# Kernel tuning notes

Measured on AMD Instinct MI355X. Metric: run time of the kernel, lower is better.

The kernel has to match this reference:

```python
import jax, jax.numpy as jnp
import numpy as np

B, S, D = 4, 4096, 256


def setup_inputs() -> dict:
    key = jax.random.key(0)
    ks = jax.random.split(key, 8)
    scale = 1.0 / np.sqrt(D)
    inp = {
        "q": jax.random.normal(ks[0], (B, S, D), jnp.float32),
        "k": jax.random.normal(ks[1], (B, S, D), jnp.float32),
        "v": jax.random.normal(ks[2], (B, S, D), jnp.float32),
        # additive mask: 1 where attention is disallowed (causal), broadcast over batch
        "mask": jnp.triu(jnp.ones((S, S), jnp.float32), k=1)[None, :, :],
        "Wq": jax.random.normal(ks[3], (D, D), jnp.float32) * scale,
        "bq": jnp.zeros((D,), jnp.float32),
        "Wk": jax.random.normal(ks[4], (D, D), jnp.float32) * scale,
        "bk": jnp.zeros((D,), jnp.float32),
        "Wv": jax.random.normal(ks[5], (D, D), jnp.float32) * scale,
        "bv": jnp.zeros((D,), jnp.float32),
        "Wo": jax.random.normal(ks[6], (D, D), jnp.float32) * scale,
        "bo": jnp.zeros((D,), jnp.float32),
    }
    return inp


def reference(q, k, v, mask, Wq, bq, Wk, bk, Wv, bv, Wo, bo):
    # Dense projections (Keras Dense: x @ W + b)
    qp = q @ Wq + bq  # [B,S,D]
    kp = k @ Wk + bk
    vp = v @ Wv + bv
    dk = jnp.asarray(qp.shape[-1], qp.dtype)
    # scaled dot-product attention, materialized scores as in the source
    logits = jnp.einsum("bqd,bkd->bqk", qp, kp) / jnp.sqrt(dk)  # [B,S,S]
    logits = logits + mask * (-1e9)
    attn = jax.nn.softmax(logits, axis=-1)  # [B,S,S]
    ctx = jnp.einsum("bqk,bkd->bqd", attn, vp)  # [B,S,D]
    z = ctx @ Wo + bo
    return z, attn
```

## Files before the change

### kernel.cpp

```cpp
#include <hip/hip_runtime.h>


typedef unsigned short u16;
typedef __attribute__((ext_vector_type(8))) short short8;
typedef __attribute__((ext_vector_type(4))) float f32x4;

struct __align__(8) us4 { u16 x, y, z, w; };

#define SEQ 4096
#define DIM 256

__device__ __forceinline__ u16 f2bf(float f) {
  unsigned int u = __float_as_uint(f);
  u += 0x7fffu + ((u >> 16) & 1u);
  return (u16)(u >> 16);
}
__device__ __forceinline__ float bf2f(u16 u) {
  return __uint_as_float(((unsigned int)u) << 16);
}

__device__ __forceinline__ void cp16(const void* g, void* l) {
  __builtin_amdgcn_global_load_lds((const __attribute__((address_space(1))) void*)g,
                                   (__attribute__((address_space(3))) void*)l, 16, 0, 0);
}

__global__ void k_wt(const float* __restrict__ Wq, const float* __restrict__ Wk,
                     const float* __restrict__ Wv, const float* __restrict__ Wo,
                     u16* __restrict__ wt) {
  __shared__ float t[32][33];
  const float* W = blockIdx.z == 0 ? Wq : blockIdx.z == 1 ? Wk : blockIdx.z == 2 ? Wv : Wo;
  u16* out = wt + (size_t)blockIdx.z * 65536;
  int n0 = blockIdx.x * 32, k0 = blockIdx.y * 32;
  int tx = threadIdx.x, ty = threadIdx.y;
  for (int i = 0; i < 4; i++)
    t[ty + i * 8][tx] = W[(size_t)(k0 + ty + i * 8) * 256 + n0 + tx];
  __syncthreads();
  for (int i = 0; i < 4; i++)
    out[(size_t)(n0 + ty + i * 8) * 256 + k0 + tx] = f2bf(t[tx][ty + i * 8]);
}

__global__ void k_pgemm3(const float* __restrict__ qin, const float* __restrict__ kin,
                         const float* __restrict__ vin, const u16* __restrict__ wtall,
                         const float* __restrict__ bq, const float* __restrict__ bk,
                         const float* __restrict__ bv,
                         u16* __restrict__ qp, u16* __restrict__ kp,
                         u16* __restrict__ vpt) {
  __shared__ __align__(16) char smem[34816];
  const int z = blockIdx.z;
  const float* A = z == 0 ? qin : z == 1 ? kin : vin;
  const u16* Wt = wtall + (size_t)z * 65536;
  const float* bias = z == 0 ? bq : z == 1 ? bk : bv;
  u16* outp = z == 0 ? qp : z == 1 ? kp : vpt;
  const bool TRANS = (z == 2);

  u16* Asm = (u16*)smem;
  u16* Bsm = Asm + 4096;
  u16* tb = (u16*)smem;
  const int tid = threadIdx.x;
  const int lane = tid & 63, w = tid >> 6;
  const int wr = w >> 1, wc = w & 1;
  const int quad = lane >> 4, m16 = lane & 15;
  const int m0 = blockIdx.y * 128, n0 = blockIdx.x * 128;

  f32x4 zero = {0.f, 0.f, 0.f, 0.f};
  f32x4 acc[4][4];
  for (int i = 0; i < 4; i++)
    for (int j = 0; j < 4; j++) acc[i][j] = zero;

  for (int kk = 0; kk < 8; ++kk) {
    const int k0 = kk * 32;
    for (int h = 0; h < 2; ++h) {
      int c = tid + h * 256;
      int row = c >> 2, sub = c & 3;
      cp16(Wt + (size_t)(n0 + row) * 256 + k0 + sub * 8, Bsm + c * 8);
    }
    for (int h = 0; h < 4; ++h) {
      int idx = h * 256 + tid;
      int row = idx >> 3, q4 = idx & 7;
      float4 a4 = *(const float4*)(A + (size_t)(m0 + row) * 256 + k0 + q4 * 4);
      us4 o;
      o.x = f2bf(a4.x); o.y = f2bf(a4.y); o.z = f2bf(a4.z); o.w = f2bf(a4.w);
      *(us4*)(Asm + row * 32 + q4 * 4) = o;
    }
    __syncthreads();
    short8 a[4], b[4];
    for (int i = 0; i < 4; ++i)
      a[i] = *(const short8*)(Asm + (wr * 64 + i * 16 + m16) * 32 + quad * 8);
    for (int j = 0; j < 4; ++j)
      b[j] = *(const short8*)(Bsm + (wc * 64 + j * 16 + m16) * 32 + quad * 8);
    for (int i = 0; i < 4; ++i)
      for (int j = 0; j < 4; ++j)
        acc[i][j] = __builtin_amdgcn_mfma_f32_16x16x32_bf16(a[i], b[j], acc[i][j], 0, 0, 0);
    __syncthreads();
  }

  if (!TRANS) {
    for (int j = 0; j < 4; ++j) {
      int gn = n0 + wc * 64 + j * 16 + m16;
      float bvx = bias[gn];
      for (int i = 0; i < 4; ++i) {
        int gm = m0 + wr * 64 + i * 16 + quad * 4;
        for (int r = 0; r < 4; ++r)
          outp[(size_t)(gm + r) * 256 + gn] = f2bf(acc[i][j][r] + bvx);
      }
    }
  } else {
    for (int j = 0; j < 4; ++j) {
      int cn = wc * 64 + j * 16 + m16;
      float bvx = bias[n0 + cn];
      for (int i = 0; i < 4; ++i) {
        int rm = wr * 64 + i * 16 + quad * 4;
        us4 o;
        o.x = f2bf(acc[i][j][0] + bvx); o.y = f2bf(acc[i][j][1] + bvx);
        o.z = f2bf(acc[i][j][2] + bvx); o.w = f2bf(acc[i][j][3] + bvx);
        *(us4*)(tb + cn * 136 + rm) = o;
      }
    }
    __syncthreads();
    int b = m0 >> 12, s0 = m0 & 4095;
    u16* dst = outp + ((size_t)b << 20);
    for (int it = 0; it < 8; ++it) {
      int idx = it * 256 + tid;
      int n = idx >> 4, m8 = idx & 15;
      short8 v8 = *(const short8*)(tb + n * 136 + m8 * 8);
      *(short8*)(dst + (size_t)(n0 + n) * 4096 + s0 + m8 * 8) = v8;
    }
  }
}

__global__ void k_qk(const u16* __restrict__ qp, const u16* __restrict__ kp,
                     u16* __restrict__ eb, float* __restrict__ attn,
                     float* __restrict__ ps) {
  int lin = blockIdx.x + (blockIdx.y << 5) + (blockIdx.z << 10);
  int wid = (lin & 7) * 512 + (lin >> 3);
  const int kt = wid & 31, qt = (wid >> 5) & 31, bz = wid >> 10;
  const int tid = threadIdx.x;
  const int q0 = qt * 128, k0t = kt * 128;

  if (kt > qt) {
    float* attnb = attn + ((size_t)bz << 24);
    f32x4 z4 = {0.f, 0.f, 0.f, 0.f};
    for (int s = 0; s < 16; ++s) {
      int idx = tid + s * 256;
      int row = idx >> 5, c4 = idx & 31;
      __builtin_nontemporal_store(z4,
          (f32x4*)(attnb + (size_t)(q0 + row) * 4096 + k0t + c4 * 4));
    }
    return;
  }

  __shared__ __align__(16) char smem[34816];
  u16* Asm = (u16*)smem;
  u16* Bsm = Asm + 4096;
  u16* epi = (u16*)smem;
  __shared__ float prow[2][128];

  const int lane = tid & 63, w = tid >> 6;
  const int wr = w >> 1, wc = w & 1;
  const int quad = lane >> 4, m16 = lane & 15;
  const u16* Ab = qp + ((size_t)bz << 20);
  const u16* Bb = kp + ((size_t)bz << 20);

  f32x4 zero = {0.f, 0.f, 0.f, 0.f};
  f32x4 acc[4][4];
  for (int i = 0; i < 4; i++)
    for (int j = 0; j < 4; j++) acc[i][j] = zero;

  for (int kk = 0; kk < 8; ++kk) {
    const int k0 = kk * 32;
    for (int h = 0; h < 2; ++h) {
      int c = tid + h * 256;
      int row = c >> 2, sub = c & 3;
      cp16(Ab + (size_t)(q0 + row) * 256 + k0 + sub * 8, Asm + c * 8);
      cp16(Bb + (size_t)(k0t + row) * 256 + k0 + sub * 8, Bsm + c * 8);
    }
    __syncthreads();
    short8 a[4], b[4];
    for (int i = 0; i < 4; ++i)
      a[i] = *(const short8*)(Asm + (wr * 64 + i * 16 + m16) * 32 + quad * 8);
    for (int j = 0; j < 4; ++j)
      b[j] = *(const short8*)(Bsm + (wc * 64 + j * 16 + m16) * 32 + quad * 8);
    for (int i = 0; i < 4; ++i)
      for (int j = 0; j < 4; ++j)
        acc[i][j] = __builtin_amdgcn_mfma_f32_16x16x32_bf16(a[i], b[j], acc[i][j], 0, 0, 0);
    __syncthreads();
  }

  float rs[4][4];
  for (int i = 0; i < 4; i++)
    for (int r = 0; r < 4; r++) rs[i][r] = 0.f;
  for (int i = 0; i < 4; ++i) {
    int gq = q0 + wr * 64 + i * 16 + quad * 4;
    for (int j = 0; j < 4; ++j) {
      int gk = k0t + wc * 64 + j * 16 + m16;
      for (int r = 0; r < 4; ++r) {
        float e = (gk <= gq + r) ? __expf(acc[i][j][r] * 0.0625f) : 0.f;
        acc[i][j][r] = e;
        rs[i][r] += e;
      }
    }
  }
  for (int off = 1; off < 16; off <<= 1)
    for (int i = 0; i < 4; ++i)
      for (int r = 0; r < 4; ++r) rs[i][r] += __shfl_xor(rs[i][r], off, 64);
  if (m16 == 0)
    for (int i = 0; i < 4; ++i)
      for (int r = 0; r < 4; ++r)
        prow[wc][wr * 64 + i * 16 + quad * 4 + r] = rs[i][r];

  for (int i = 0; i < 4; ++i)
    for (int j = 0; j < 4; ++j) {
      int rl = wr * 64 + i * 16 + quad * 4;
      int cl = wc * 64 + j * 16 + m16;
      for (int r = 0; r < 4; ++r) epi[(rl + r) * 136 + cl] = f2bf(acc[i][j][r]);
    }
  __syncthreads();

  u16* ebt = eb + ((size_t)bz * 528 + (size_t)(qt * (qt + 1) / 2 + kt)) * 16384;
  for (int it = 0; it < 8; ++it) {
    int idx = it * 256 + tid;
    int row = idx >> 4, m8 = idx & 15;
    short8 v8 = *(const short8*)(epi + row * 136 + m8 * 8);
    *(short8*)(ebt + row * 128 + m8 * 8) = v8;
  }
  if (tid < 128)
    ps[(size_t)(bz * 32 + kt) * 4096 + q0 + tid] = prow[0][tid] + prow[1][tid];
}

__global__ void __launch_bounds__(256) k_pv2(const u16* __restrict__ eb,
                                             const u16* __restrict__ vpt,
                                             const float* __restrict__ ps,
                                             float* __restrict__ attn,
                                             float* __restrict__ ctxf) {
  int lin = blockIdx.x + (blockIdx.y << 3) + (blockIdx.z << 8);
  int wid = (lin & 7) * 128 + (lin >> 3);
  const int nh = wid & 1, kg = (wid >> 1) & 3;
  const int qt = (wid >> 3) & 31, bz = wid >> 8;
  const int nt_lo = (kg * (qt + 1)) >> 2;
  const int nt_hi = ((kg + 1) * (qt + 1)) >> 2;
  if (nt_lo >= nt_hi) return;

  __shared__ u16 A_lds[2][128 * 64];
  __shared__ u16 B_lds[2][128 * 64];
  __shared__ float inv_lds[128];

  const int tid = threadIdx.x;
  const int lane = tid & 63, w = tid >> 6;
  const int wr = w >> 1, wc = w & 1;
  const int quad = lane >> 4, m16 = lane & 15;
  const int q0 = qt * 128;
  const u16* ebq = eb + ((size_t)bz * 528 + (size_t)(qt * (qt + 1) / 2)) * 16384;
  float* attnb = attn + ((size_t)bz << 24);
  const u16* vb = vpt + ((size_t)bz << 20) + (size_t)nh * 128 * 4096;

  if (tid < 128) {
    float s = 0.f;
    for (int kt = 0; kt <= qt; ++kt)
      s += ps[(size_t)(bz * 32 + kt) * 4096 + q0 + tid];
    inv_lds[tid] = 1.f / s;
  }

  short8 arg[4], brg[4];
  const int sc = tid & 7;
  int srow[4], soff[4];
  for (int t = 0; t < 4; ++t) {
    srow[t] = (t * 256 + tid) >> 3;
    soff[t] = srow[t] * 64 + ((((sc << 4) ^ ((srow[t] & 7) << 4))) >> 1);
  }

  auto stage_load = [&](int hh) {
    int t0 = nt_lo + (hh >> 1), h = hh & 1;
    const u16* tile = ebq + (size_t)t0 * 16384 + h * 64;
    int kt0 = t0 * 128 + h * 64;
    for (int t = 0; t < 4; ++t) {
      arg[t] = *(const short8*)(tile + srow[t] * 128 + sc * 8);
      brg[t] = *(const short8*)(vb + (size_t)srow[t] * 4096 + kt0 + sc * 8);
    }
  };
  auto stage_write = [&](int buf) {
    for (int t = 0; t < 4; ++t) {
      *(short8*)(A_lds[buf] + soff[t]) = arg[t];
      *(short8*)(B_lds[buf] + soff[t]) = brg[t];
    }
  };

  const int khalves = (nt_hi - nt_lo) * 2;
  stage_load(0);
  stage_write(0);
  __syncthreads();

  f32x4 zero = {0.f, 0.f, 0.f, 0.f};
  f32x4 acc[4][4];
  for (int i = 0; i < 4; i++)
    for (int j = 0; j < 4; j++) acc[i][j] = zero;

  for (int hh = 0; hh < khalves; ++hh) {
    const int buf = hh & 1;
    if (hh + 1 < khalves) stage_load(hh + 1);

    for (int p = 0; p < 4; ++p) {
      int idx = p * 256 + tid;
      int rl = idx >> 3, c8 = idx & 7;
      int lb = rl * 64 + ((((c8 << 4) ^ ((rl & 7) << 4))) >> 1);
      short8 e8 = *(const short8*)(A_lds[buf] + lb);
      float ivr = inv_lds[rl];
      f32x4 lo, hi;
      for (int t = 0; t < 4; ++t) lo[t] = bf2f((u16)e8[t]) * ivr;
      for (int t = 0; t < 4; ++t) hi[t] = bf2f((u16)e8[t + 4]) * ivr;
      int kcol = (nt_lo + (hh >> 1)) * 128 + (hh & 1) * 64 + (c8 << 3);
      float* dst = attnb + (size_t)(q0 + rl) * 4096 + kcol;
      __builtin_nontemporal_store(lo, (f32x4*)dst);
      __builtin_nontemporal_store(hi, (f32x4*)(dst + 4));
    }

    for (int ks = 0; ks < 2; ++ks) {
      short8 a[4], b[4];
      for (int i = 0; i < 4; ++i) {
        int row = wr * 64 + i * 16 + m16;
        int xb = (ks * 64 + quad * 16) ^ ((row & 7) << 4);
        a[i] = *(const short8*)(A_lds[buf] + row * 64 + (xb >> 1));
      }
      for (int j = 0; j < 4; ++j) {
        int n = wc * 64 + j * 16 + m16;
        int xb = (ks * 64 + quad * 16) ^ ((n & 7) << 4);
        b[j] = *(const short8*)(B_lds[buf] + n * 64 + (xb >> 1));
      }
      for (int i = 0; i < 4; ++i)
        for (int j = 0; j < 4; ++j)
          acc[i][j] = __builtin_amdgcn_mfma_f32_16x16x32_bf16(a[i], b[j], acc[i][j], 0, 0, 0);
    }

    if (hh + 1 < khalves) stage_write(buf ^ 1);
    __syncthreads();
  }

  float* ctxs = ctxf + ((size_t)(kg * 4 + bz) << 20);
  for (int i = 0; i < 4; ++i) {
    int rl = wr * 64 + i * 16 + quad * 4;
    for (int j = 0; j < 4; ++j) {
      int gn = nh * 128 + wc * 64 + j * 16 + m16;
      for (int r = 0; r < 4; ++r)
        ctxs[(size_t)(q0 + rl + r) * 256 + gn] = acc[i][j][r] * inv_lds[rl + r];
    }
  }
}

__global__ void k_cvt(const float* __restrict__ ctxf, u16* __restrict__ ctx) {
  size_t i4 = (size_t)blockIdx.x * 256 + threadIdx.x;
  int bz = (int)(i4 >> 18);
  size_t rem4 = i4 & (((size_t)1 << 18) - 1);
  int qrow = (int)(rem4 >> 6);
  int qt = qrow >> 7;
  const float4* base = (const float4*)ctxf;
  float4 s = make_float4(0.f, 0.f, 0.f, 0.f);
  for (int kg = 0; kg < 4; ++kg) {
    if ((((kg + 1) * (qt + 1)) >> 2) > ((kg * (qt + 1)) >> 2)) {
      float4 t = base[((size_t)(kg * 4 + bz) << 18) + rem4];
      s.x += t.x; s.y += t.y; s.z += t.z; s.w += t.w;
    }
  }
  us4 o;
  o.x = f2bf(s.x); o.y = f2bf(s.y); o.z = f2bf(s.z); o.w = f2bf(s.w);
  ((us4*)ctx)[i4] = o;
}

template <bool OUT_BF16>
__global__ void k_gemm(const u16* __restrict__ A, const u16* __restrict__ Wt,
                       const float* __restrict__ bias, void* __restrict__ outp) {
  __shared__ u16 Asm[128 * 32];
  __shared__ u16 Bsm[128 * 32];
  const int tid = threadIdx.x;
  const int lane = tid & 63, w = tid >> 6;
  const int wr = w >> 1, wc = w & 1;
  const int quad = lane >> 4, m16 = lane & 15;
  const int m0 = blockIdx.y * 128, n0 = blockIdx.x * 128;

  f32x4 zero = {0.f, 0.f, 0.f, 0.f};
  f32x4 acc[4][4];
  for (int i = 0; i < 4; i++)
    for (int j = 0; j < 4; j++) acc[i][j] = zero;

  for (int kk = 0; kk < 8; ++kk) {
    const int k0 = kk * 32;
    for (int h = 0; h < 2; ++h) {
      int c = tid + h * 256;
      int row = c >> 2, sub = c & 3;
      cp16(A + (size_t)(m0 + row) * 256 + k0 + sub * 8, Asm + c * 8);
      cp16(Wt + (size_t)(n0 + row) * 256 + k0 + sub * 8, Bsm + c * 8);
    }
    __syncthreads();
    short8 a[4], b[4];
    for (int i = 0; i < 4; ++i)
      a[i] = *(const short8*)(Asm + (wr * 64 + i * 16 + m16) * 32 + quad * 8);
    for (int j = 0; j < 4; ++j)
      b[j] = *(const short8*)(Bsm + (wc * 64 + j * 16 + m16) * 32 + quad * 8);
    for (int i = 0; i < 4; ++i)
      for (int j = 0; j < 4; ++j)
        acc[i][j] = __builtin_amdgcn_mfma_f32_16x16x32_bf16(a[i], b[j], acc[i][j], 0, 0, 0);
    __syncthreads();
  }

  for (int j = 0; j < 4; ++j) {
    int gn = n0 + wc * 64 + j * 16 + m16;
    float bv = bias[gn];
    for (int i = 0; i < 4; ++i) {
      int gm = m0 + wr * 64 + i * 16 + quad * 4;
      for (int r = 0; r < 4; ++r) {
        float val = acc[i][j][r] + bv;
        if (OUT_BF16)
          ((u16*)outp)[(size_t)(gm + r) * 256 + gn] = f2bf(val);
        else
          ((float*)outp)[(size_t)(gm + r) * 256 + gn] = val;
      }
    }
  }
}

extern "C" void kernel_launch(void* const* d_in, const int* in_sizes, int n_in,
                              void* d_out, int out_size, void* d_ws, size_t ws_size,
                              hipStream_t stream) {
  const float* q  = (const float*)d_in[0];
  const float* k  = (const float*)d_in[1];
  const float* v  = (const float*)d_in[2];
  const float* Wq = (const float*)d_in[4];
  const float* bq = (const float*)d_in[5];
  const float* Wk = (const float*)d_in[6];
  const float* bk = (const float*)d_in[7];
  const float* Wv = (const float*)d_in[8];
  const float* bv = (const float*)d_in[9];
  const float* Wo = (const float*)d_in[10];
  const float* bo = (const float*)d_in[11];

  const size_t MD = (size_t)16384 * 256;
  u16* qp  = (u16*)d_ws;
  u16* kp  = qp + MD;
  u16* vpt = kp + MD;
  u16* ctx = vpt + MD;
  u16* wt  = ctx + MD;
  float* ps   = (float*)(wt + 4 * 65536);
  float* ctxf = ps + (size_t)4 * 32 * 4096;
  u16* eb = (u16*)(ctxf + (size_t)16 * 1024 * 1024);

  float* zout = (float*)d_out;
  float* attn = zout + (size_t)4 * 4096 * 256;

  k_wt<<<dim3(8, 8, 4), dim3(32, 8), 0, stream>>>(Wq, Wk, Wv, Wo, wt);
  k_pgemm3<<<dim3(2, 128, 3), 256, 0, stream>>>(q, k, v, wt, bq, bk, bv, qp, kp, vpt);
  k_qk<<<dim3(32, 32, 4), 256, 0, stream>>>(qp, kp, eb, attn, ps);
  k_pv2<<<dim3(8, 32, 4), 256, 0, stream>>>(eb, vpt, ps, attn, ctxf);
  k_cvt<<<4096, 256, 0, stream>>>(ctxf, ctx);
  k_gemm<false><<<dim3(2, 128), 256, 0, stream>>>(ctx, wt + 3 * 65536, bo, zout);
}
```

Before: 494.2 us.

## Register-prefetch QK tiles with XOR-swizzled LDS and 64-wide k steps

Rewrites the QK^T main loop in k_qk. It now prefetches the next 64-wide k-slice of Q and K into registers while MFMAs run on the current slice in LDS, replacing the synchronous 32-wide global_load_lds copies. LDS rows are XOR-swizzled to avoid bank conflicts on the short8 fragment reads, and launch_bounds(256,3) is added to cap registers for occupancy. The cost is extra registers for the prefetch buffers and a larger LDS tile.

```diff
diff --git a/kernel.cpp b/kernel.cpp
--- a/kernel.cpp
+++ b/kernel.cpp
@@ -128,9 +128,11 @@
   }
 }
 
-__global__ void k_qk(const u16* __restrict__ qp, const u16* __restrict__ kp,
-                     u16* __restrict__ eb, float* __restrict__ attn,
-                     float* __restrict__ ps) {
+__global__ void __launch_bounds__(256, 3) k_qk(const u16* __restrict__ qp,
+                                               const u16* __restrict__ kp,
+                                               u16* __restrict__ eb,
+                                               float* __restrict__ attn,
+                                               float* __restrict__ ps) {
   int lin = blockIdx.x + (blockIdx.y << 5) + (blockIdx.z << 10);
   int wid = (lin & 7) * 512 + (lin >> 3);
   const int kt = wid & 31, qt = (wid >> 5) & 31, bz = wid >> 10;
@@ -150,8 +152,8 @@
   }
 
   __shared__ __align__(16) char smem[34816];
-  u16* Asm = (u16*)smem;
-  u16* Bsm = Asm + 4096;
+  u16* A_lds = (u16*)smem;
+  u16* B_lds = A_lds + 8192;
   u16* epi = (u16*)smem;
   __shared__ float prow[2][128];
 
@@ -161,29 +163,60 @@
   const u16* Ab = qp + ((size_t)bz << 20);
   const u16* Bb = kp + ((size_t)bz << 20);
 
+  short8 arg[4], brg[4];
+  const int sc = tid & 7;
+  int srow[4], soff[4];
+  for (int t = 0; t < 4; ++t) {
+    srow[t] = (t * 256 + tid) >> 3;
+    soff[t] = srow[t] * 64 + ((((sc << 4) ^ ((srow[t] & 7) << 4))) >> 1);
+  }
+
+  auto stage_load = [&](int kk) {
+    const int k0 = kk * 64;
+    for (int t = 0; t < 4; ++t) {
+      arg[t] = *(const short8*)(Ab + (size_t)(q0 + srow[t]) * 256 + k0 + sc * 8);
+      brg[t] = *(const short8*)(Bb + (size_t)(k0t + srow[t]) * 256 + k0 + sc * 8);
+    }
+  };
+  auto stage_write = [&]() {
+    for (int t = 0; t < 4; ++t) {
+      *(short8*)(A_lds + soff[t]) = arg[t];
+      *(short8*)(B_lds + soff[t]) = brg[t];
+    }
+  };
+
   f32x4 zero = {0.f, 0.f, 0.f, 0.f};
   f32x4 acc[4][4];
   for (int i = 0; i < 4; i++)
     for (int j = 0; j < 4; j++) acc[i][j] = zero;
 
-  for (int kk = 0; kk < 8; ++kk) {
-    const int k0 = kk * 32;
-    for (int h = 0; h < 2; ++h) {
-      int c = tid + h * 256;
-      int row = c >> 2, sub = c & 3;
-      cp16(Ab + (size_t)(q0 + row) * 256 + k0 + sub * 8, Asm + c * 8);
-      cp16(Bb + (size_t)(k0t + row) * 256 + k0 + sub * 8, Bsm + c * 8);
-    }
-    __syncthreads();
-    short8 a[4], b[4];
-    for (int i = 0; i < 4; ++i)
-      a[i] = *(const short8*)(Asm + (wr * 64 + i * 16 + m16) * 32 + quad * 8);
-    for (int j = 0; j < 4; ++j)
-      b[j] = *(const short8*)(Bsm + (wc * 64 + j * 16 + m16) * 32 + quad * 8);
-    for (int i = 0; i < 4; ++i)
-      for (int j = 0; j < 4; ++j)
-        acc[i][j] = __builtin_amdgcn_mfma_f32_16x16x32_bf16(a[i], b[j], acc[i][j], 0, 0, 0);
-    __syncthreads();
+  stage_load(0);
+  stage_write();
+  __syncthreads();
+
+  for (int kk = 0; kk < 4; ++kk) {
+    if (kk + 1 < 4) stage_load(kk + 1);
+    for (int ks = 0; ks < 2; ++ks) {
+      short8 a[4], b[4];
+      for (int i = 0; i < 4; ++i) {
+        int row = wr * 64 + i * 16 + m16;
+        int xb = (ks * 64 + quad * 16) ^ ((row & 7) << 4);
+        a[i] = *(const short8*)(A_lds + row * 64 + (xb >> 1));
+      }
+      for (int j = 0; j < 4; ++j) {
+        int n = wc * 64 + j * 16 + m16;
+        int xb = (ks * 64 + quad * 16) ^ ((n & 7) << 4);
+        b[j] = *(const short8*)(B_lds + n * 64 + (xb >> 1));
+      }
+      for (int i = 0; i < 4; ++i)
+        for (int j = 0; j < 4; ++j)
+          acc[i][j] = __builtin_amdgcn_mfma_f32_16x16x32_bf16(a[i], b[j], acc[i][j], 0, 0, 0);
+    }
+    __syncthreads();
+    if (kk + 1 < 4) {
+      stage_write();
+      __syncthreads();
+    }
   }
 
   float rs[4][4];
```

Result: no change. 494.6 us (median of 2 runs) (+0.1%).
